# Performance work log

Hardware: AMD Instinct MI355X
Metric: run time of the kernel (lower is better)

## Reference

```python
import jax, jax.numpy as jnp
import numpy as np
from jax import lax

VOCAB = 256
H = 1024
L = 2
B = 64
T = 512
RESIDUAL = True


def setup_inputs() -> dict:
    key = jax.random.key(0)
    ks = jax.random.split(key, 8)
    s_ih = 1.0 / np.sqrt(H)
    return {
        "X": jax.random.randint(ks[0], (B, T), 0, VOCAB),
        "embed": jax.random.normal(ks[1], (VOCAB, H), dtype=jnp.float32) * 0.02,
        "Wih": jax.random.normal(ks[2], (L, 4 * H, H), dtype=jnp.float32) * s_ih,
        "Whh": jax.random.normal(ks[3], (L, 4 * H, H), dtype=jnp.float32) * s_ih,
        "bih": jax.random.normal(ks[4], (L, 4 * H), dtype=jnp.float32) * s_ih,
        "bhh": jax.random.normal(ks[5], (L, 4 * H), dtype=jnp.float32) * s_ih,
        "Wout": jax.random.normal(ks[6], (VOCAB, H), dtype=jnp.float32) * s_ih,
        "bout": jax.random.normal(ks[7], (VOCAB,), dtype=jnp.float32) * s_ih,
    }


def reference(X, embed, Wih, Whh, bih, bhh, Wout, bout):
    # X: [B, T] int tokens. Original loops over t in [0, T-2]: feeds X[:, t]
    # through an L-layer (residual) LSTM one char at a time, accumulates
    # mean-over-batch cross entropy vs X[:, t+1], then divides by T.
    Bsz, Tlen = X.shape
    n_layers = Wih.shape[0]
    xs = embed[X[:, :-1]]          # [B, T-1, H] embedded inputs
    xs_t = jnp.swapaxes(xs, 0, 1)  # [T-1, B, H] time-major for scan

    def cell(carry, x_t):
        h, c = carry  # each [L, B, H]
        inp = x_t
        hs, cs = [], []
        for l in range(n_layers):
            # torch LSTM gate order: input, forget, cell(g), output
            gates = inp @ Wih[l].T + h[l] @ Whh[l].T + (bih[l] + bhh[l])
            i_g, f_g, g_g, o_g = jnp.split(gates, 4, axis=-1)
            c_l = jax.nn.sigmoid(f_g) * c[l] + jax.nn.sigmoid(i_g) * jnp.tanh(g_g)
            h_l = jax.nn.sigmoid(o_g) * jnp.tanh(c_l)
            hs.append(h_l)
            cs.append(c_l)
            inp = h_l + inp if RESIDUAL else h_l
        return (jnp.stack(hs), jnp.stack(cs)), inp

    init = (jnp.zeros((n_layers, Bsz, xs.shape[-1]), xs.dtype),
            jnp.zeros((n_layers, Bsz, xs.shape[-1]), xs.dtype))
    _, outs = lax.scan(cell, init, xs_t)       # [T-1, B, H]

    logits = outs @ Wout.T + bout              # [T-1, B, V]
    targets = X[:, 1:].T                        # [T-1, B]
    logp = jax.nn.log_softmax(logits, axis=-1)
    ce = -jnp.take_along_axis(logp, targets[..., None], axis=-1)[..., 0]  # [T-1, B]
    loss = ce.mean(axis=1).sum() / Tlen
    return loss
```

## Files before the change

### kernel.cpp

```cpp
#include <hip/hip_runtime.h>
#include <hip/hip_bf16.h>

typedef __hip_bfloat16 bf16;
typedef short v8s __attribute__((ext_vector_type(8)));
typedef float v4f __attribute__((ext_vector_type(4)));
typedef float v16f __attribute__((ext_vector_type(16)));
typedef unsigned long long u64;

static __device__ __forceinline__ float bf2f(bf16 x) { return __bfloat162float(x); }
static __device__ __forceinline__ unsigned short bfbits(float f) {
    bf16 t = __float2bfloat16(f);
    return *(unsigned short*)&t;
}
static __device__ __forceinline__ float fast_tanh(float x) {
    float e = __expf(-2.f * x);
    return (1.f - e) / (1.f + e);
}

__global__ __launch_bounds__(256) void k_zero(float* __restrict__ zbase, float* __restrict__ loss) {
    int idx = blockIdx.x * 256 + threadIdx.x;
    if (idx < 140288) zbase[idx] = 0.0f;
    if (idx == 0) loss[0] = 0.0f;
}

__global__ __launch_bounds__(256) void k_convert_w(const float* __restrict__ Wih,
                                                   const float* __restrict__ Whh,
                                                   bf16* __restrict__ Wb) {
    int idx = blockIdx.x * 256 + threadIdx.x;
    int k2 = idx & 2047;
    int ln = idx >> 11;
    float v = (k2 < 1024) ? Wih[ln * 1024 + k2] : Whh[ln * 1024 + (k2 - 1024)];
    Wb[idx] = __float2bfloat16(v);
}

__global__ __launch_bounds__(256) void k_convert_small(const float* __restrict__ Wout,
                                                       const float* __restrict__ bih,
                                                       const float* __restrict__ bhh,
                                                       bf16* __restrict__ Wob,
                                                       float* __restrict__ bsum) {
    int idx = blockIdx.x * 256 + threadIdx.x;
    if (idx < 262144) Wob[idx] = __float2bfloat16(Wout[idx]);
    int bidx = idx - 262144;
    if (bidx >= 0 && bidx < 8192) bsum[bidx] = bih[bidx] + bhh[bidx];
}

__global__ __launch_bounds__(256) void k_embed(const int* __restrict__ X,
                                               const float* __restrict__ embed,
                                               bf16* __restrict__ x0) {
    int bi = blockIdx.x;
    int kc = bi & 3;
    int tb = bi >> 2;
    int b  = tb & 63;
    int t  = tb >> 6;
    int k  = kc * 256 + threadIdx.x;
    int tok = X[b * 512 + t];
    x0[(long)tb * 1024 + k] = __float2bfloat16(embed[tok * 1024 + k]);
}

#define GLDI_C(dst, p, o) asm volatile("global_load_dwordx4 %0, %1, off offset:%2"     : "=v"(dst) : "v"(p), "i"(o))
#define GLDI_B(dst, p, o) asm volatile("global_load_dwordx4 %0, %1, off offset:%2 sc1" : "=v"(dst) : "v"(p), "i"(o))
#define MFMA(acc, a, w) asm volatile("v_mfma_f32_32x32x16_bf16 %0, %1, %2, %0" : "+v"(acc) : "v"(a), "a"(w))
#define VW(n)  asm volatile("s_waitcnt vmcnt(%0)" :: "i"(n))
#define VW0()  asm volatile("s_waitcnt vmcnt(0)")
#define ZACC(a) do { _Pragma("unroll") for (int r_ = 0; r_ < 16; ++r_) a[r_] = 0.f; } while(0)

#define ISSUE(GLD, c, B) do { \
    GLD(B[0], pA0, (c)*128 +  0); GLD(B[1], pA1, (c)*128 +  0); \
    GLD(B[2], pA0, (c)*128 + 32); GLD(B[3], pA1, (c)*128 + 32); \
    GLD(B[4], pA0, (c)*128 + 64); GLD(B[5], pA1, (c)*128 + 64); \
    GLD(B[6], pA0, (c)*128 + 96); GLD(B[7], pA1, (c)*128 + 96); } while(0)

#define CHUNK(c, B) do { _Pragma("unroll") for (int i_ = 0; i_ < 4; ++i_) { \
    MFMA(acc00, B[2*i_],   wa0[(c)*4+i_]); \
    MFMA(acc10, B[2*i_+1], wa0[(c)*4+i_]); \
    MFMA(acc01, B[2*i_],   wa1[(c)*4+i_]); \
    MFMA(acc11, B[2*i_+1], wa1[(c)*4+i_]); } } while(0)

#define PIPE(GLD) do { \
    ISSUE(GLD,0,bufa); ISSUE(GLD,1,bufb); ISSUE(GLD,2,bufc); ISSUE(GLD,3,bufd); \
    VW(24); CHUNK(0,bufa); ISSUE(GLD,4,bufa); \
    VW(24); CHUNK(1,bufb); ISSUE(GLD,5,bufb); \
    VW(24); CHUNK(2,bufc); ISSUE(GLD,6,bufc); \
    VW(24); CHUNK(3,bufd); ISSUE(GLD,7,bufd); \
    VW(24); CHUNK(4,bufa); \
    VW(16); CHUNK(5,bufb); \
    VW(8);  CHUNK(6,bufc); \
    VW(0);  CHUNK(7,bufd); } while(0)

#define WRGP(OP) do { _Pragma("unroll") for (int r_ = 0; r_ < 16; ++r_) { \
    const int grow_ = (r_&3) + ((r_>>2)<<3) + ((l>>5)<<2); \
    gp[q&1][grow_][l&31]          OP acc00[r_]; \
    gp[q&1][grow_][32+(l&31)]     OP acc01[r_]; \
    gp[q&1][32+grow_][l&31]       OP acc10[r_]; \
    gp[q&1][32+grow_][32+(l&31)]  OP acc11[r_]; } } while(0)

__global__ __launch_bounds__(256, 1) void k_lstm(bf16* __restrict__ x0all,
                                                 bf16* __restrict__ x1buf,
                                                 bf16* __restrict__ h0buf,
                                                 bf16* __restrict__ h1buf,
                                                 const bf16* __restrict__ Wb,
                                                 const float* __restrict__ bsum,
                                                 unsigned* bar) {
    __shared__ float gp[2][64][67];
    __shared__ float c_lds[64][17];
    __shared__ float b_lds[64];

    const int g     = blockIdx.x;
    const int layer = g >> 6;
    const int j     = g & 63;
    const int tid   = threadIdx.x;
    const int l     = tid & 63;
    const int q     = tid >> 6;

    unsigned* myline = bar + ((layer << 3) + (j & 7)) * 32;

    if (tid < 64) b_lds[tid] = bsum[layer * 4096 + (tid >> 4) * 1024 + (j << 4) + (tid & 15)];
    for (int i = tid; i < 64 * 17; i += 256) ((float*)c_lds)[i] = 0.f;

    const int nl0 = l & 31, nl1 = 32 + (l & 31);
    const long N0 = (long)((nl0 >> 4) * 1024 + (j << 4) + (nl0 & 15));
    const long N1 = (long)((nl1 >> 4) * 1024 + (j << 4) + (nl1 & 15));
    const bf16* wp0 = Wb + (long)layer * 8388608 + N0 * 2048 + q * 512 + ((l >> 5) << 3);
    const bf16* wp1 = Wb + (long)layer * 8388608 + N1 * 2048 + q * 512 + ((l >> 5) << 3);
    v8s wa0[32], wa1[32];
#pragma unroll
    for (int kk = 0; kk < 32; ++kk) {
        wa0[kk] = *(const v8s*)(wp0 + kk * 16);
        asm volatile("" : "+a"(wa0[kk]));
        wa1[kk] = *(const v8s*)(wp1 + kk * 16);
        asm volatile("" : "+a"(wa1[kk]));
    }

    const int ab = tid >> 2;
    const int dq = tid & 3;
    const int off_ = ab * 1024 + (j << 4) + dq * 4;
    const bool prewave = (layer == 0) && (q < 2);

    int s3 = 0;

#pragma unroll 1
    for (int s = 0; s < 512; ++s) {
        const bool act = (layer == 0) ? (s < 511) : (s >= 1);
        const int s3p = (s3 == 0) ? 2 : s3 - 1;
        const bf16* xop = x0all + (long)s * 65536;
        const bf16* x1p = x1buf + s3p * 65536;
        const bf16* h0p = h0buf + ((s + 1) & 1) * 65536;
        const bf16* h1p = h1buf + ((s + 1) & 1) * 65536;
        bf16* hdst  = (layer ? h1buf : h0buf) + (s & 1) * 65536;
        bf16* x1dst = x1buf + s3 * 65536;
        bf16* res1  = x0all + (long)(s - 1) * 65536;

        const bf16* base = (layer == 0) ? ((q < 2) ? xop : h0p)
                                        : ((q < 2) ? x1p : h1p);
        const bf16* pA0 = base + ((q & 1) << 9) + (l & 31) * 1024 + ((l >> 5) << 3);
        const bf16* pA1 = pA0 + 32 * 1024;

        v16f acc00, acc01, acc10, acc11;
        v8s bufa[8], bufb[8], bufc[8], bufd[8];
        u64 xv = 0;

        if (act && layer == 0) xv = *(const u64*)(xop + off_);
        if (act && prewave) {
            ZACC(acc00); ZACC(acc01); ZACC(acc10); ZACC(acc11);
            PIPE(GLDI_C);
            WRGP(=);
        }
        if (s > 0 && q == 0) {
            unsigned req = 0;
            if (l < 16)
                req = (layer == 0 && l >= 8) ? (8u * (unsigned)s - 8u) : (8u * (unsigned)s);
            const unsigned* lp = bar + l * 32;
            for (;;) {
                unsigned v = req;
                if (l < 16)
                    asm volatile("global_load_dword %0, %1, off sc1\n\t"
                                 "s_waitcnt vmcnt(0)" : "=v"(v) : "v"(lp));
                if (__ballot(v >= req) == ~0ull) break;
            }
        }
        __syncthreads();
        if (act && !prewave) {
            if (layer == 1) {
                const bf16* xrp = x1p + off_;
                asm volatile("global_load_dwordx2 %0, %1, off sc1" : "=v"(xv) : "v"(xrp));
            }
            ZACC(acc00); ZACC(acc01); ZACC(acc10); ZACC(acc11);
            PIPE(GLDI_B);
            if (q < 2) WRGP(=);
        }
        __syncthreads();
        if (act && q >= 2) WRGP(+=);
        __syncthreads();

        if (act) {
            float hv4[4];
#pragma unroll
            for (int i = 0; i < 4; ++i) {
                const int d = dq * 4 + i;
                const float gi = gp[0][ab][d]      + gp[1][ab][d]      + b_lds[d];
                const float gf = gp[0][ab][16 + d] + gp[1][ab][16 + d] + b_lds[16 + d];
                const float gg = gp[0][ab][32 + d] + gp[1][ab][32 + d] + b_lds[32 + d];
                const float go = gp[0][ab][48 + d] + gp[1][ab][48 + d] + b_lds[48 + d];
                const float si = 1.f / (1.f + __expf(-gi));
                const float sf = 1.f / (1.f + __expf(-gf));
                const float so = 1.f / (1.f + __expf(-go));
                const float tg = fast_tanh(gg);
                const float cn = sf * c_lds[ab][d] + si * tg;
                c_lds[ab][d] = cn;
                hv4[i] = so * fast_tanh(cn);
            }
            u64 hv64 = 0, rv64 = 0;
#pragma unroll
            for (int i = 0; i < 4; ++i) {
                const unsigned us = (unsigned)((xv >> (16 * i)) & 0xffffu);
                const float rv = hv4[i] + __uint_as_float(us << 16);
                hv64 |= (u64)bfbits(hv4[i]) << (16 * i);
                rv64 |= (u64)bfbits(rv) << (16 * i);
            }
            bf16* hp = hdst + off_;
            asm volatile("global_store_dwordx2 %0, %1, off sc1" :: "v"(hp), "v"(hv64) : "memory");
            bf16* rp = (layer == 0) ? (x1dst + off_) : (res1 + off_);
            asm volatile("global_store_dwordx2 %0, %1, off sc1" :: "v"(rp), "v"(rv64) : "memory");
        }
        VW0();
        __syncthreads();
        if (tid == 0)
            __hip_atomic_fetch_add(myline, 1u, __ATOMIC_RELAXED, __HIP_MEMORY_SCOPE_AGENT);
        s3 = (s3 == 2) ? 0 : s3 + 1;
    }
}

__global__ __launch_bounds__(256) void k_final(const bf16* __restrict__ outAll,
                                               const bf16* __restrict__ Wob,
                                               const float* __restrict__ bout,
                                               const int* __restrict__ X,
                                               float* __restrict__ loss) {
    const int t    = blockIdx.x;
    const int tid  = threadIdx.x;
    const int lane = tid & 63;
    const int w    = tid >> 6;
    const int col  = lane & 15;
    const int oct  = lane >> 4;
    const bf16* arow = outAll + ((long)t * 64 + (w << 4) + col) * 1024 + (oct << 3);
    v4f acc[16];
#pragma unroll
    for (int nt = 0; nt < 16; ++nt) acc[nt] = (v4f){0.f, 0.f, 0.f, 0.f};
    for (int k0 = 0; k0 < 1024; k0 += 32) {
        v8s a = *(const v8s*)(arow + k0);
#pragma unroll
        for (int nt = 0; nt < 16; ++nt) {
            v8s bb = *(const v8s*)(Wob + ((nt << 4) + col) * 1024 + (oct << 3) + k0);
            acc[nt] = __builtin_amdgcn_mfma_f32_16x16x32_bf16(a, bb, acc[nt], 0, 0, 0);
        }
    }
#pragma unroll
    for (int nt = 0; nt < 16; ++nt) {
        const float bb = bout[(nt << 4) + col];
        acc[nt][0] += bb; acc[nt][1] += bb; acc[nt][2] += bb; acc[nt][3] += bb;
    }
    float ce_sum = 0.f;
#pragma unroll
    for (int r = 0; r < 4; ++r) {
        float mx = -3.4e38f;
#pragma unroll
        for (int nt = 0; nt < 16; ++nt) mx = fmaxf(mx, acc[nt][r]);
#pragma unroll
        for (int mm = 1; mm < 16; mm <<= 1) mx = fmaxf(mx, __shfl_xor(mx, mm, 64));
        float ss = 0.f;
#pragma unroll
        for (int nt = 0; nt < 16; ++nt) ss += __expf(acc[nt][r] - mx);
#pragma unroll
        for (int mm = 1; mm < 16; mm <<= 1) ss += __shfl_xor(ss, mm, 64);
        const int b   = (w << 4) + (oct << 2) + r;
        const int tok = X[b * 512 + t + 1];
        float lt = 0.f;
#pragma unroll
        for (int nt = 0; nt < 16; ++nt)
            if ((tok >> 4) == nt) lt = acc[nt][r];
        if ((tok & 15) == col)
            ce_sum += mx + __logf(ss) - lt;
    }
#pragma unroll
    for (int mm = 1; mm < 64; mm <<= 1) ce_sum += __shfl_xor(ce_sum, mm, 64);
    if (lane == 0) atomicAdd(loss, ce_sum * (1.0f / 32768.0f));
}

extern "C" void kernel_launch(void* const* d_in, const int* in_sizes, int n_in,
                              void* d_out, int out_size, void* d_ws, size_t ws_size,
                              hipStream_t stream) {
    const int*   X     = (const int*)  d_in[0];
    const float* embed = (const float*)d_in[1];
    const float* Wih   = (const float*)d_in[2];
    const float* Whh   = (const float*)d_in[3];
    const float* bih   = (const float*)d_in[4];
    const float* bhh   = (const float*)d_in[5];
    const float* Wout  = (const float*)d_in[6];
    const float* bout  = (const float*)d_in[7];
    float* loss = (float*)d_out;

    char* ws = (char*)d_ws;
    bf16*     x0all = (bf16*)(ws + 0);
    bf16*     Wb    = (bf16*)(ws + 66977792);
    bf16*     Wob   = (bf16*)(ws + 100532224);
    bf16*     x1buf = (bf16*)(ws + 101056512);
    bf16*     h0buf = (bf16*)(ws + 101449728);
    bf16*     h1buf = (bf16*)(ws + 101711872);
    float*    bsum  = (float*)(ws + 101974016);
    unsigned* bar   = (unsigned*)(ws + 102006784);
    float*    zbase = (float*)(ws + 101449728);

    if (ws_size < 102010880u) return;

    k_zero<<<548, 256, 0, stream>>>(zbase, loss);
    k_convert_w<<<65536, 256, 0, stream>>>(Wih, Whh, Wb);
    k_convert_small<<<1056, 256, 0, stream>>>(Wout, bih, bhh, Wob, bsum);
    k_embed<<<130816, 256, 0, stream>>>(X, embed, x0all);

    void* args[] = {&x0all, &x1buf, &h0buf, &h1buf, &Wb, &bsum, &bar};
    hipLaunchCooperativeKernel((void*)k_lstm, dim3(128), dim3(256), args, 0, stream);

    k_final<<<511, 256, 0, stream>>>(x0all, Wob, bout, X, loss);
}
```

Before: 6.028 ms.

## Replace atomic-counter barrier with per-block stamps and per-wave dependency polling

Each block now writes its step number to its own stamp line instead of incrementing a shared atomic counter. Each wave polls only the 32 producer blocks whose data it actually reads, so it can start its half of the matmul without a block-wide barrier before compute. The residual input load moves to after the gate reduction. This aims to cut barrier latency and atomic contention on the per-timestep critical path of the recurrent loop. In exchange, every wave runs its own polling loop and correctness depends on the new ordering of stamps relative to the buffers they guard.

After: 5.848 ms. -3.0%, faster.

```diff
diff --git a/kernel.cpp b/kernel.cpp
--- a/kernel.cpp
+++ b/kernel.cpp
@@ -19,7 +19,7 @@
 
 __global__ __launch_bounds__(256) void k_zero(float* __restrict__ zbase, float* __restrict__ loss) {
     int idx = blockIdx.x * 256 + threadIdx.x;
-    if (idx < 140288) zbase[idx] = 0.0f;
+    if (idx < 143360) zbase[idx] = 0.0f;
     if (idx == 0) loss[0] = 0.0f;
 }
 
@@ -94,13 +94,23 @@
     gp[q&1][32+grow_][l&31]       OP acc10[r_]; \
     gp[q&1][32+grow_][32+(l&31)]  OP acc11[r_]; } } while(0)
 
+#define POLL(baseidx, req) do { \
+    const unsigned* sp_ = stamps + ((baseidx) + (l & 31)) * 32; \
+    for (;;) { \
+        int v_ = (req); \
+        if (l < 32) \
+            asm volatile("global_load_dword %0, %1, off sc1\n\t" \
+                         "s_waitcnt vmcnt(0)" : "=v"(v_) : "v"(sp_)); \
+        if (__ballot(v_ >= (req)) == ~0ull) break; \
+    } } while(0)
+
 __global__ __launch_bounds__(256, 1) void k_lstm(bf16* __restrict__ x0all,
                                                  bf16* __restrict__ x1buf,
                                                  bf16* __restrict__ h0buf,
                                                  bf16* __restrict__ h1buf,
                                                  const bf16* __restrict__ Wb,
                                                  const float* __restrict__ bsum,
-                                                 unsigned* bar) {
+                                                 unsigned* stamps) {
     __shared__ float gp[2][64][67];
     __shared__ float c_lds[64][17];
     __shared__ float b_lds[64];
@@ -112,8 +122,6 @@
     const int l     = tid & 63;
     const int q     = tid >> 6;
 
-    unsigned* myline = bar + ((layer << 3) + (j & 7)) * 32;
-
     if (tid < 64) b_lds[tid] = bsum[layer * 4096 + (tid >> 4) * 1024 + (j << 4) + (tid & 15)];
     for (int i = tid; i < 64 * 17; i += 256) ((float*)c_lds)[i] = 0.f;
 
@@ -135,6 +143,11 @@
     const int dq = tid & 3;
     const int off_ = ab * 1024 + (j << 4) + dq * 4;
     const bool prewave = (layer == 0) && (q < 2);
+    const int pbase = (layer == 0)
+                      ? ((q < 2) ? 64 + ((q & 1) << 5)
+                                 : ((q & 1) << 5))
+                      : ((q < 2) ? ((q & 1) << 5)
+                                 : 64 + ((q & 1) << 5));
 
     int s3 = 0;
 
@@ -159,40 +172,36 @@
         v8s bufa[8], bufb[8], bufc[8], bufd[8];
         u64 xv = 0;
 
-        if (act && layer == 0) xv = *(const u64*)(xop + off_);
-        if (act && prewave) {
-            ZACC(acc00); ZACC(acc01); ZACC(acc10); ZACC(acc11);
-            PIPE(GLDI_C);
-            WRGP(=);
-        }
-        if (s > 0 && q == 0) {
-            unsigned req = 0;
-            if (l < 16)
-                req = (layer == 0 && l >= 8) ? (8u * (unsigned)s - 8u) : (8u * (unsigned)s);
-            const unsigned* lp = bar + l * 32;
-            for (;;) {
-                unsigned v = req;
-                if (l < 16)
-                    asm volatile("global_load_dword %0, %1, off sc1\n\t"
-                                 "s_waitcnt vmcnt(0)" : "=v"(v) : "v"(lp));
-                if (__ballot(v >= req) == ~0ull) break;
+        if (act) {
+            if (prewave) {
+                xv = *(const u64*)(xop + off_);
+                ZACC(acc00); ZACC(acc01); ZACC(acc10); ZACC(acc11);
+                PIPE(GLDI_C);
+                WRGP(=);
+                if (s > 0) POLL(pbase, s - 1);
+            } else {
+                if (s > 0) POLL(pbase, s);
+                if (layer == 1 && q < 2) {
+                    if (q == 0) xv = *(const u64*)(xop + off_);
+                    const bf16* xrp = x1p + off_;
+                    asm volatile("global_load_dwordx2 %0, %1, off sc1" : "=v"(xv) : "v"(xrp));
+                }
+                ZACC(acc00); ZACC(acc01); ZACC(acc10); ZACC(acc11);
+                PIPE(GLDI_B);
+                if (q < 2) WRGP(=);
             }
-        }
-        __syncthreads();
-        if (act && !prewave) {
-            if (layer == 1) {
-                const bf16* xrp = x1p + off_;
-                asm volatile("global_load_dwordx2 %0, %1, off sc1" : "=v"(xv) : "v"(xrp));
-            }
-            ZACC(acc00); ZACC(acc01); ZACC(acc10); ZACC(acc11);
-            PIPE(GLDI_B);
-            if (q < 2) WRGP(=);
         }
         __syncthreads();
         if (act && q >= 2) WRGP(+=);
         __syncthreads();
 
         if (act) {
+            if (layer == 0) xv = *(const u64*)(xop + off_);
+            else {
+                const bf16* xrp = x1p + off_;
+                asm volatile("global_load_dwordx2 %0, %1, off sc1\n\t"
+                             "s_waitcnt vmcnt(0)" : "=v"(xv) : "v"(xrp));
+            }
             float hv4[4];
 #pragma unroll
             for (int i = 0; i < 4; ++i) {
@@ -224,8 +233,11 @@
         }
         VW0();
         __syncthreads();
-        if (tid == 0)
-            __hip_atomic_fetch_add(myline, 1u, __ATOMIC_RELAXED, __HIP_MEMORY_SCOPE_AGENT);
+        if (tid == 0) {
+            unsigned* sp = stamps + g * 32;
+            int sv = s + 1;
+            asm volatile("global_store_dword %0, %1, off sc1" :: "v"(sp), "v"(sv) : "memory");
+        }
         s3 = (s3 == 2) ? 0 : s3 + 1;
     }
 }
@@ -299,24 +311,24 @@
     float* loss = (float*)d_out;
 
     char* ws = (char*)d_ws;
-    bf16*     x0all = (bf16*)(ws + 0);
-    bf16*     Wb    = (bf16*)(ws + 66977792);
-    bf16*     Wob   = (bf16*)(ws + 100532224);
-    bf16*     x1buf = (bf16*)(ws + 101056512);
-    bf16*     h0buf = (bf16*)(ws + 101449728);
-    bf16*     h1buf = (bf16*)(ws + 101711872);
-    float*    bsum  = (float*)(ws + 101974016);
-    unsigned* bar   = (unsigned*)(ws + 102006784);
-    float*    zbase = (float*)(ws + 101449728);
-
-    if (ws_size < 102010880u) return;
-
-    k_zero<<<548, 256, 0, stream>>>(zbase, loss);
+    bf16*     x0all  = (bf16*)(ws + 0);
+    bf16*     Wb     = (bf16*)(ws + 66977792);
+    bf16*     Wob    = (bf16*)(ws + 100532224);
+    bf16*     x1buf  = (bf16*)(ws + 101056512);
+    bf16*     h0buf  = (bf16*)(ws + 101449728);
+    bf16*     h1buf  = (bf16*)(ws + 101711872);
+    float*    bsum   = (float*)(ws + 101974016);
+    unsigned* stamps = (unsigned*)(ws + 102006784);
+    float*    zbase  = (float*)(ws + 101449728);
+
+    if (ws_size < 102023168u) return;
+
+    k_zero<<<560, 256, 0, stream>>>(zbase, loss);
     k_convert_w<<<65536, 256, 0, stream>>>(Wih, Whh, Wb);
     k_convert_small<<<1056, 256, 0, stream>>>(Wout, bih, bhh, Wob, bsum);
     k_embed<<<130816, 256, 0, stream>>>(X, embed, x0all);
 
-    void* args[] = {&x0all, &x1buf, &h0buf, &h1buf, &Wb, &bsum, &bar};
+    void* args[] = {&x0all, &x1buf, &h0buf, &h1buf, &Wb, &bsum, &stamps};
     hipLaunchCooperativeKernel((void*)k_lstm, dim3(128), dim3(256), args, 0, stream);
 
     k_final<<<511, 256, 0, stream>>>(x0all, Wob, bout, X, loss);
```
